# Kernel tuning notes

Measured on AMD Instinct MI355X. Metric: run time of the kernel, lower is better.

## Reference

```python
import jax, jax.numpy as jnp
import numpy as np

B, N, F = 32, 1024, 128

def setup_inputs() -> dict:
    key = jax.random.key(0)
    k1, k2, k3, k4 = jax.random.split(key, 4)
    adjMs = jax.random.uniform(k1, (B, N, N), dtype=jnp.float32)
    feats = jax.random.normal(k2, (B, N, F), dtype=jnp.float32)
    w = jax.random.normal(k3, (F, F), dtype=jnp.float32) * 0.05  # random_normal init scale
    b = jax.random.normal(k4, (1,), dtype=jnp.float32)
    return {"adjMs": adjMs, "feats": feats, "w": w, "b": b}

def reference(adjMs, feats, w, b):
    # adj[b,i,j] = feats[b,i] @ w @ feats[b,j] + b  (bilinear form V W V^T + b)
    vw = jnp.einsum('bnf,fg->bng', feats, w)          # [B,N,F]
    y = jnp.einsum('bng,bmg->bnm', vw, feats) + b[0]  # [B,N,N]
    # activation = 'linear' (identity); invertProb=False so no inversion branch
    return (y, feats)
```

## Files before the change

### kernel.cpp

```cpp
#include <hip/hip_runtime.h>

#define Bsz 32
#define Nn  1024
#define Ff  128

typedef __attribute__((ext_vector_type(8))) short bf16x8;
typedef __attribute__((ext_vector_type(4))) float f32x4;
typedef __attribute__((ext_vector_type(4))) short s16x4;

static __device__ inline short f2bf(float f) {
    unsigned u = __builtin_bit_cast(unsigned, f);
    unsigned r = u + 0x7FFFu + ((u >> 16) & 1u);
    return (short)(r >> 16);
}

__global__ __launch_bounds__(256) void prep_kernel(
    const float* __restrict__ feats,
    const float* __restrict__ w,
    float* __restrict__ out_feats,
    short* __restrict__ feats_bf,
    short* __restrict__ wT_bf)
{
    int gid = blockIdx.x * blockDim.x + threadIdx.x;
    const int total4 = Bsz * Nn * Ff / 4;
    if (gid < total4) {
        float4 v = ((const float4*)feats)[gid];
        ((float4*)out_feats)[gid] = v;
        s16x4 s;
        s.x = f2bf(v.x); s.y = f2bf(v.y); s.z = f2bf(v.z); s.w = f2bf(v.w);
        ((s16x4*)feats_bf)[gid] = s;
    }
    if (gid < Ff * Ff) {
        int g = gid >> 7, k = gid & 127;
        wT_bf[gid] = f2bf(w[k * Ff + g]);
    }
}

__global__ __launch_bounds__(256) void gemm1_kernel(
    const float* __restrict__ feats,
    const short* __restrict__ wT,
    short* __restrict__ vw)
{
    const int row0 = blockIdx.x * 64;
    const int tid  = threadIdx.x;
    const int wid  = tid >> 6;
    const int lane = tid & 63;
    const int wm = wid >> 1, wn = wid & 1;
    const int lr = lane & 15;
    const int kg = lane >> 4;

    const int wrow0 = row0 + wm * 32;
    const int wg0   = wn * 64;

    f32x4 acc[2][4] = {};

    for (int kc = 0; kc < 4; ++kc) {
        int k0 = kc * 32 + kg * 8;
        bf16x8 a[2], b[4];
        for (int mf = 0; mf < 2; ++mf) {
            const float* p = feats + (size_t)(wrow0 + mf * 16 + lr) * Ff + k0;
            float4 v0 = ((const float4*)p)[0];
            float4 v1 = ((const float4*)p)[1];
            a[mf] = (bf16x8){ f2bf(v0.x), f2bf(v0.y), f2bf(v0.z), f2bf(v0.w),
                              f2bf(v1.x), f2bf(v1.y), f2bf(v1.z), f2bf(v1.w) };
        }
        for (int nf = 0; nf < 4; ++nf) {
            const short* p = wT + (size_t)(wg0 + nf * 16 + lr) * Ff + k0;
            b[nf] = *((const bf16x8*)p);
        }
        for (int mf = 0; mf < 2; ++mf)
            for (int nf = 0; nf < 4; ++nf)
                acc[mf][nf] = __builtin_amdgcn_mfma_f32_16x16x32_bf16(
                    a[mf], b[nf], acc[mf][nf], 0, 0, 0);
    }

    for (int mf = 0; mf < 2; ++mf) {
        int row = wrow0 + mf * 16 + kg * 4;
        for (int nf = 0; nf < 4; ++nf) {
            int g = wg0 + nf * 16 + lr;
            for (int r = 0; r < 4; ++r)
                vw[(size_t)(row + r) * Ff + g] = f2bf(acc[mf][nf][r]);
        }
    }
}

__global__ __launch_bounds__(256) void gemm2_kernel(
    const short* __restrict__ vw,
    const short* __restrict__ fb,
    const float* __restrict__ bias,
    float* __restrict__ y)
{
    int blk  = blockIdx.x;
    int bidx = blk >> 6;
    int t    = blk & 63;
    int mt = t >> 3, nt = t & 7;
    int tid = threadIdx.x;
    int wid = tid >> 6, lane = tid & 63;
    int wm = wid >> 1, wn = wid & 1;
    int lr = lane & 15, kg = lane >> 4;

    const short* A  = vw + (size_t)bidx * Nn * Ff;
    const short* Bp = fb + (size_t)bidx * Nn * Ff;
    int am0 = mt * 128 + wm * 64;
    int bn0 = nt * 128 + wn * 64;

    f32x4 acc[4][4] = {};

    for (int kc = 0; kc < 4; ++kc) {
        int k0 = kc * 32 + kg * 8;
        bf16x8 a[4], b[4];
        for (int mf = 0; mf < 4; ++mf)
            a[mf] = *((const bf16x8*)(A + (size_t)(am0 + mf * 16 + lr) * Ff + k0));
        for (int nf = 0; nf < 4; ++nf)
            b[nf] = *((const bf16x8*)(Bp + (size_t)(bn0 + nf * 16 + lr) * Ff + k0));
        for (int mf = 0; mf < 4; ++mf)
            for (int nf = 0; nf < 4; ++nf)
                acc[mf][nf] = __builtin_amdgcn_mfma_f32_16x16x32_bf16(
                    a[mf], b[nf], acc[mf][nf], 0, 0, 0);
    }

    float bv = bias[0];
    float* Y = y + (size_t)bidx * Nn * Nn;
    for (int mf = 0; mf < 4; ++mf) {
        int row = am0 + mf * 16 + kg * 4;
        for (int nf = 0; nf < 4; ++nf) {
            int col = bn0 + nf * 16 + lr;
            float* p = Y + (size_t)row * Nn + col;
            for (int r = 0; r < 4; ++r)
                p[(size_t)r * Nn] = acc[mf][nf][r] + bv;
        }
    }
}

extern "C" void kernel_launch(void* const* d_in, const int* in_sizes, int n_in,
                              void* d_out, int out_size, void* d_ws, size_t ws_size,
                              hipStream_t stream) {
    const float* feats = (const float*)d_in[1];
    const float* w     = (const float*)d_in[2];
    const float* bias  = (const float*)d_in[3];
    float* y = (float*)d_out;
    float* out_feats = y + (size_t)Bsz * Nn * Nn;

    short* vw = (short*)d_ws;
    short* fb = vw + (size_t)Bsz * Nn * Ff;
    short* wT = fb + (size_t)Bsz * Nn * Ff;

    prep_kernel<<<4096, 256, 0, stream>>>(feats, w, out_feats, fb, wT);
    gemm1_kernel<<<512, 256, 0, stream>>>(feats, wT, vw);
    gemm2_kernel<<<32 * 64, 256, 0, stream>>>(vw, fb, bias, y);
}
```

Baseline: 65.80 us.

## Fuse feats copy and bf16 cast into gemm1, vectorize gemm2 stores, XCD-aware mapping

The feats copy-out and bf16 conversion move out of the prep kernel and into the first GEMM, so feats is read once, and the prep kernel now only transposes W. In the second GEMM the operands are swapped (B as the A-operand), so each lane holds four consecutive columns and writes one 16-byte store instead of four strided scalar stores. Blocks are also remapped so that each XCD handles four whole batches, which aims to keep each batch's operands in one L2. The main cost being attacked is the 128MB output write and the extra pass over feats.

```diff
diff --git a/kernel.cpp b/kernel.cpp
--- a/kernel.cpp
+++ b/kernel.cpp
@@ -6,7 +6,6 @@
 
 typedef __attribute__((ext_vector_type(8))) short bf16x8;
 typedef __attribute__((ext_vector_type(4))) float f32x4;
-typedef __attribute__((ext_vector_type(4))) short s16x4;
 
 static __device__ inline short f2bf(float f) {
     unsigned u = __builtin_bit_cast(unsigned, f);
@@ -14,86 +13,72 @@
     return (short)(r >> 16);
 }
 
-__global__ __launch_bounds__(256) void prep_kernel(
-    const float* __restrict__ feats,
-    const float* __restrict__ w,
-    float* __restrict__ out_feats,
-    short* __restrict__ feats_bf,
-    short* __restrict__ wT_bf)
+__global__ __launch_bounds__(256) void k0_wt(
+    const float* __restrict__ w, short* __restrict__ wT)
 {
     int gid = blockIdx.x * blockDim.x + threadIdx.x;
-    const int total4 = Bsz * Nn * Ff / 4;
-    if (gid < total4) {
-        float4 v = ((const float4*)feats)[gid];
-        ((float4*)out_feats)[gid] = v;
-        s16x4 s;
-        s.x = f2bf(v.x); s.y = f2bf(v.y); s.z = f2bf(v.z); s.w = f2bf(v.w);
-        ((s16x4*)feats_bf)[gid] = s;
-    }
     if (gid < Ff * Ff) {
         int g = gid >> 7, k = gid & 127;
-        wT_bf[gid] = f2bf(w[k * Ff + g]);
+        wT[gid] = f2bf(w[k * Ff + g]);
     }
 }
 
-__global__ __launch_bounds__(256) void gemm1_kernel(
+__global__ __launch_bounds__(256) void k1_fused(
     const float* __restrict__ feats,
     const short* __restrict__ wT,
+    float* __restrict__ out_feats,
+    short* __restrict__ fb,
     short* __restrict__ vw)
 {
     const int row0 = blockIdx.x * 64;
     const int tid  = threadIdx.x;
     const int wid  = tid >> 6;
     const int lane = tid & 63;
-    const int wm = wid >> 1, wn = wid & 1;
     const int lr = lane & 15;
     const int kg = lane >> 4;
 
-    const int wrow0 = row0 + wm * 32;
-    const int wg0   = wn * 64;
+    const int myrow = row0 + wid * 16 + lr;
+    const float* frow = feats + (size_t)myrow * Ff;
+    float* orow       = out_feats + (size_t)myrow * Ff;
+    short* brow       = fb + (size_t)myrow * Ff;
 
-    f32x4 acc[2][4] = {};
+    f32x4 acc[8] = {};
 
     for (int kc = 0; kc < 4; ++kc) {
         int k0 = kc * 32 + kg * 8;
-        bf16x8 a[2], b[4];
-        for (int mf = 0; mf < 2; ++mf) {
-            const float* p = feats + (size_t)(wrow0 + mf * 16 + lr) * Ff + k0;
-            float4 v0 = ((const float4*)p)[0];
-            float4 v1 = ((const float4*)p)[1];
-            a[mf] = (bf16x8){ f2bf(v0.x), f2bf(v0.y), f2bf(v0.z), f2bf(v0.w),
-                              f2bf(v1.x), f2bf(v1.y), f2bf(v1.z), f2bf(v1.w) };
+        float4 v0 = ((const float4*)(frow + k0))[0];
+        float4 v1 = ((const float4*)(frow + k0))[1];
+        ((float4*)(orow + k0))[0] = v0;
+        ((float4*)(orow + k0))[1] = v1;
+        bf16x8 a = (bf16x8){ f2bf(v0.x), f2bf(v0.y), f2bf(v0.z), f2bf(v0.w),
+                             f2bf(v1.x), f2bf(v1.y), f2bf(v1.z), f2bf(v1.w) };
+        *((bf16x8*)(brow + k0)) = a;
+        for (int nf = 0; nf < 8; ++nf) {
+            bf16x8 b = *((const bf16x8*)(wT + (size_t)(nf * 16 + lr) * Ff + k0));
+            acc[nf] = __builtin_amdgcn_mfma_f32_16x16x32_bf16(a, b, acc[nf], 0, 0, 0);
         }
-        for (int nf = 0; nf < 4; ++nf) {
-            const short* p = wT + (size_t)(wg0 + nf * 16 + lr) * Ff + k0;
-            b[nf] = *((const bf16x8*)p);
-        }
-        for (int mf = 0; mf < 2; ++mf)
-            for (int nf = 0; nf < 4; ++nf)
-                acc[mf][nf] = __builtin_amdgcn_mfma_f32_16x16x32_bf16(
-                    a[mf], b[nf], acc[mf][nf], 0, 0, 0);
     }
 
-    for (int mf = 0; mf < 2; ++mf) {
-        int row = wrow0 + mf * 16 + kg * 4;
-        for (int nf = 0; nf < 4; ++nf) {
-            int g = wg0 + nf * 16 + lr;
-            for (int r = 0; r < 4; ++r)
-                vw[(size_t)(row + r) * Ff + g] = f2bf(acc[mf][nf][r]);
-        }
+    for (int nf = 0; nf < 8; ++nf) {
+        int g = nf * 16 + lr;
+        for (int r = 0; r < 4; ++r)
+            vw[(size_t)(row0 + wid * 16 + kg * 4 + r) * Ff + g] = f2bf(acc[nf][r]);
     }
 }
 
-__global__ __launch_bounds__(256) void gemm2_kernel(
+__global__ __launch_bounds__(256) void k2_gemm2(
     const short* __restrict__ vw,
     const short* __restrict__ fb,
     const float* __restrict__ bias,
     float* __restrict__ y)
 {
     int blk  = blockIdx.x;
-    int bidx = blk >> 6;
-    int t    = blk & 63;
+    int xcd  = blk & 7;
+    int idx  = blk >> 3;
+    int bidx = xcd * 4 + (idx >> 6);
+    int t    = idx & 63;
     int mt = t >> 3, nt = t & 7;
+
     int tid = threadIdx.x;
     int wid = tid >> 6, lane = tid & 63;
     int wm = wid >> 1, wn = wid & 1;
@@ -113,21 +98,24 @@
             a[mf] = *((const bf16x8*)(A + (size_t)(am0 + mf * 16 + lr) * Ff + k0));
         for (int nf = 0; nf < 4; ++nf)
             b[nf] = *((const bf16x8*)(Bp + (size_t)(bn0 + nf * 16 + lr) * Ff + k0));
-        for (int mf = 0; mf < 4; ++mf)
-            for (int nf = 0; nf < 4; ++nf)
-                acc[mf][nf] = __builtin_amdgcn_mfma_f32_16x16x32_bf16(
-                    a[mf], b[nf], acc[mf][nf], 0, 0, 0);
+        for (int nf = 0; nf < 4; ++nf)
+            for (int mf = 0; mf < 4; ++mf)
+                acc[nf][mf] = __builtin_amdgcn_mfma_f32_16x16x32_bf16(
+                    b[nf], a[mf], acc[nf][mf], 0, 0, 0);
     }
 
     float bv = bias[0];
     float* Y = y + (size_t)bidx * Nn * Nn;
+
     for (int mf = 0; mf < 4; ++mf) {
-        int row = am0 + mf * 16 + kg * 4;
+        float* rowp = Y + (size_t)(am0 + mf * 16 + lr) * Nn + bn0 + kg * 4;
         for (int nf = 0; nf < 4; ++nf) {
-            int col = bn0 + nf * 16 + lr;
-            float* p = Y + (size_t)row * Nn + col;
-            for (int r = 0; r < 4; ++r)
-                p[(size_t)r * Nn] = acc[mf][nf][r] + bv;
+            f32x4 v;
+            v[0] = acc[nf][mf][0] + bv;
+            v[1] = acc[nf][mf][1] + bv;
+            v[2] = acc[nf][mf][2] + bv;
+            v[3] = acc[nf][mf][3] + bv;
+            *((f32x4*)(rowp + nf * 16)) = v;
         }
     }
 }
@@ -145,7 +133,7 @@
     short* fb = vw + (size_t)Bsz * Nn * Ff;
     short* wT = fb + (size_t)Bsz * Nn * Ff;
 
-    prep_kernel<<<4096, 256, 0, stream>>>(feats, w, out_feats, fb, wT);
-    gemm1_kernel<<<512, 256, 0, stream>>>(feats, wT, vw);
-    gemm2_kernel<<<32 * 64, 256, 0, stream>>>(vw, fb, bias, y);
+    k0_wt<<<64, 256, 0, stream>>>(w, wT);
+    k1_fused<<<512, 256, 0, stream>>>(feats, wT, out_feats, fb, vw);
+    k2_gemm2<<<2048, 256, 0, stream>>>(vw, fb, bias, y);
 }
```

Measured after the change: 69.97 us. 1.06x slower.
